# Performance work log

Hardware: AMD Instinct MI355X
Metric: run time of the kernel (lower is better)

The kernel has to match this reference:

```python
import jax, jax.numpy as jnp
import numpy as np

N = 50000          # num nodes
E = 800000         # num edges (avg degree 16)
D_IN, D_H, D_OUT = 128, 64, 64
HS, NC = 128, 10   # lstm hidden_size, num_classes


def setup_inputs() -> dict:
    key = jax.random.key(0)
    ks = jax.random.split(key, 20)
    s = 0.05
    rn = lambda k, shape: (jax.random.normal(k, shape, dtype=jnp.float32) * s)
    inp = {
        "x": jax.random.normal(ks[0], (N, D_IN), dtype=jnp.float32),
        "edge_index": jax.random.randint(ks[1], (2, E), 0, N, dtype=jnp.int64),
        # GCN layer weights (PyG GCNConv: lin has no bias; separate additive bias)
        "W1": rn(ks[2], (D_IN, D_H)), "b1": jnp.zeros((D_H,), jnp.float32),
        "W2": rn(ks[3], (D_H, D_H)), "b2": jnp.zeros((D_H,), jnp.float32),
        "W3": rn(ks[4], (D_H, D_H)), "b3": jnp.zeros((D_H,), jnp.float32),
        "W4": rn(ks[5], (D_H, D_H)), "b4": jnp.zeros((D_H,), jnp.float32),
        "W5": rn(ks[6], (D_H, D_OUT)), "b5": jnp.zeros((D_OUT,), jnp.float32),
        # LSTM (gate order i, f, g, o as in torch.nn.LSTM)
        "W_ih": rn(ks[7], (4 * HS, D_OUT)), "W_hh": rn(ks[8], (4 * HS, HS)),
        "b_ih": jnp.zeros((4 * HS,), jnp.float32), "b_hh": jnp.zeros((4 * HS,), jnp.float32),
        # FC head
        "W_fc": rn(ks[9], (NC, HS)), "b_fc": jnp.zeros((NC,), jnp.float32),
    }
    return inp


def reference(x, edge_index, W1, b1, W2, b2, W3, b3, W4, b4, W5, b5,
              W_ih, W_hh, b_ih, b_hh, W_fc, b_fc):
    n = x.shape[0]
    # add self loops (PyG GCNConv default)
    loops = jnp.arange(n, dtype=edge_index.dtype)
    row = jnp.concatenate([edge_index[0], loops])  # source nodes
    col = jnp.concatenate([edge_index[1], loops])  # target nodes
    # symmetric normalization D^{-1/2} (A+I) D^{-1/2}
    deg = jax.ops.segment_sum(jnp.ones_like(col, dtype=x.dtype), col, num_segments=n)
    dinv = jnp.where(deg > 0, jax.lax.rsqrt(deg), 0.0)
    norm = dinv[row] * dinv[col]                   # [E+N]

    def conv(h, W, b):
        h = h @ W                                  # [N, d_out]
        msg = h[row] * norm[:, None]               # gather + scale  [E+N, d_out]
        return jax.ops.segment_sum(msg, col, num_segments=n) + b

    h = jax.nn.relu(conv(x, W1, b1))
    h = jax.nn.relu(conv(h, W2, b2))
    h = jax.nn.relu(conv(h, W3, b3))
    h = jax.nn.relu(conv(h, W4, b4))
    h = jax.nn.relu(conv(h, W5, b5))               # [N, D_OUT]

    # single-timestep LSTM (seq_len=1, batch=N, h0=c0=0), gate order i,f,g,o
    hs = W_hh.shape[1]
    h0 = jnp.zeros((n, hs), x.dtype)
    c0 = jnp.zeros((n, hs), x.dtype)
    gates = h @ W_ih.T + h0 @ W_hh.T + b_ih + b_hh  # [N, 4*HS]
    i, f, g, o = jnp.split(gates, 4, axis=1)
    i = jax.nn.sigmoid(i); f = jax.nn.sigmoid(f)
    g = jnp.tanh(g);       o = jax.nn.sigmoid(o)
    c1 = f * c0 + i * g
    h1 = o * jnp.tanh(c1)                           # [N, HS]
    return h1 @ W_fc.T + b_fc                       # [N, NC]
```

## Files before the change

### kernel.cpp

```cpp
#include <hip/hip_runtime.h>
#include <math.h>

#define DOUT 64


__global__ __launch_bounds__(256) void k_count(const int* __restrict__ col,
                                               int* __restrict__ cnt, int e) {
    int i = blockIdx.x * 256 + threadIdx.x;
    if (i < e) atomicAdd(&cnt[col[i]], 1);
}


__global__ __launch_bounds__(256) void k_scanA(const int* __restrict__ cnt,
                                               int* __restrict__ bsum, int n) {
    __shared__ int part[256];
    const int t = threadIdx.x;
    const int base = blockIdx.x * 1024 + t * 4;
    int s = 0;
    #pragma unroll
    for (int i = 0; i < 4; i++) { int idx = base + i; if (idx < n) s += cnt[idx]; }
    part[t] = s;
    __syncthreads();
    #pragma unroll
    for (int off = 128; off > 0; off >>= 1) {
        if (t < off) part[t] += part[t + off];
        __syncthreads();
    }
    if (t == 0) bsum[blockIdx.x] = part[0];
}

__global__ __launch_bounds__(64) void k_scanB(const int* __restrict__ bsum,
                                              int* __restrict__ boff, int nb) {
    const int t = threadIdx.x;
    int val = (t < nb) ? bsum[t] : 0;
    const int own = val;
    #pragma unroll
    for (int off = 1; off < 64; off <<= 1) {
        int v = __shfl_up(val, off);
        if (t >= off) val += v;
    }
    if (t < nb) boff[t] = val - own;
}

__global__ __launch_bounds__(256) void k_scanC(const int* __restrict__ cnt,
                                               const int* __restrict__ boff,
                                               int* __restrict__ rowptr,
                                               int* __restrict__ cursor,
                                               float* __restrict__ dinv,
                                               int n, int e_total) {
    __shared__ int part[256];
    const int t = threadIdx.x;
    const int base = blockIdx.x * 1024 + t * 4;
    int c[4];
    int s = 0;
    #pragma unroll
    for (int i = 0; i < 4; i++) {
        int idx = base + i;
        c[i] = (idx < n) ? cnt[idx] : 0;
        s += c[i];
    }
    part[t] = s;
    __syncthreads();
    for (int off = 1; off < 256; off <<= 1) {
        int v = 0;
        if (t >= off) v = part[t - off];
        __syncthreads();
        if (t >= off) part[t] += v;
        __syncthreads();
    }
    int run = boff[blockIdx.x] + ((t > 0) ? part[t - 1] : 0);
    #pragma unroll
    for (int i = 0; i < 4; i++) {
        int idx = base + i;
        if (idx < n) {
            rowptr[idx] = run;
            cursor[idx] = run;
            dinv[idx] = rsqrtf((float)(c[i] + 1));
            run += c[i];
        }
    }
    if (blockIdx.x == 0 && t == 0) rowptr[n] = e_total;
}

__global__ __launch_bounds__(256) void k_fill(const int* __restrict__ row,
                                              const int* __restrict__ col,
                                              int* __restrict__ cursor,
                                              int* __restrict__ srcidx, int e) {
    int i = blockIdx.x * 256 + threadIdx.x;
    if (i < e) {
        int p = atomicAdd(&cursor[col[i]], 1);
        srcidx[p] = row[i];
    }
}

__global__ __launch_bounds__(256) void k_transp(const float* __restrict__ W1,
                                                const float* __restrict__ W2,
                                                const float* __restrict__ W3,
                                                const float* __restrict__ W4,
                                                const float* __restrict__ W5,
                                                float* __restrict__ WT) {
    int i = blockIdx.x * 256 + threadIdx.x;
    if (i < 8192) {
        int j = i >> 7, d = i & 127;
        WT[i] = W1[d * 64 + j];
    } else if (i < 24576) {
        int q = i - 8192;
        int w = q >> 12, r = q & 4095;
        int j = r >> 6, d = r & 63;
        const float* Ws = (w == 0) ? W2 : (w == 1) ? W3 : (w == 2) ? W4 : W5;
        WT[i] = Ws[d * 64 + j];
    }
}

template<int D, bool RELU>
__global__ __launch_bounds__(256) void k_gemm2(const float* __restrict__ X,
                                               const float* __restrict__ WT,
                                               const float* __restrict__ dinv,
                                               float* __restrict__ hWs, int n) {
    constexpr int D4 = D / 4;
    __shared__ float Wls[64 * D];
    __shared__ float Xls[32 * D];
    const int t = threadIdx.x;
    const int node0 = blockIdx.x * 32;
    float4* Wl4 = (float4*)Wls;
    float4* Xl4 = (float4*)Xls;

    for (int i = t; i < 64 * D4; i += 256) {
        int r = i / D4, d4 = i % D4;
        Wl4[r * D4 + (d4 ^ (((r >> 4) & 3) << 2))] = ((const float4*)WT)[i];
    }
    for (int i = t; i < 32 * D4; i += 256) {
        int nd = i / D4, d4 = i % D4;
        float4 v = make_float4(0.f, 0.f, 0.f, 0.f);
        int node = node0 + nd;
        if (node < n) {
            v = ((const float4*)X)[(size_t)node * D4 + d4];
            if (RELU) {
                v.x = fmaxf(v.x, 0.f); v.y = fmaxf(v.y, 0.f);
                v.z = fmaxf(v.z, 0.f); v.w = fmaxf(v.w, 0.f);
            }
            float di = dinv[node];
            v.x *= di; v.y *= di; v.z *= di; v.w *= di;
        }
        Xl4[i] = v;
    }
    __syncthreads();

    const int wv = t >> 6, lane = t & 63;
    const int swz = ((lane >> 4) & 3) << 2;
    float acc[8];
    #pragma unroll
    for (int q = 0; q < 8; q++) acc[q] = 0.f;

    #pragma unroll 4
    for (int d4 = 0; d4 < D4; d4++) {
        float4 w = Wl4[lane * D4 + (d4 ^ swz)];
        #pragma unroll
        for (int q = 0; q < 8; q++) {
            float4 xv = Xl4[(wv * 8 + q) * D4 + d4];
            acc[q] = fmaf(xv.w, w.w, fmaf(xv.z, w.z, fmaf(xv.y, w.y, fmaf(xv.x, w.x, acc[q]))));
        }
    }
    #pragma unroll
    for (int q = 0; q < 8; q++) {
        int node = node0 + wv * 8 + q;
        if (node < n) hWs[(size_t)node * 64 + lane] = acc[q];
    }
}

__global__ __launch_bounds__(256) void k_gather(const int* __restrict__ rowptr,
                                                const int* __restrict__ srcidx,
                                                const float* __restrict__ dinv,
                                                const float* __restrict__ b,
                                                const float* __restrict__ hWs,
                                                float* __restrict__ agg, int n) {
    const int t = threadIdx.x;
    int w = (blockIdx.x * 256 + t) >> 6;
    if (w >= n) return;
    w = __builtin_amdgcn_readfirstlane(w);
    const int lane = t & 63;
    const int f4 = lane & 15;
    const int es = lane >> 4;
    const float4* H4 = (const float4*)hWs;
    const int s = rowptr[w], e = rowptr[w + 1];
    float4 acc = make_float4(0.f, 0.f, 0.f, 0.f);
    if (es == 0) acc = H4[(size_t)w * 16 + f4];
    for (int i = s + es; i < e; i += 4) {
        int src = srcidx[i];
        float4 v = H4[(size_t)src * 16 + f4];
        acc.x += v.x; acc.y += v.y; acc.z += v.z; acc.w += v.w;
    }
    #pragma unroll
    for (int off = 16; off < 64; off <<= 1) {
        acc.x += __shfl_xor(acc.x, off);
        acc.y += __shfl_xor(acc.y, off);
        acc.z += __shfl_xor(acc.z, off);
        acc.w += __shfl_xor(acc.w, off);
    }
    if (es == 0) {
        float di = dinv[w];
        float4 bv = ((const float4*)b)[f4];
        float4 o;
        o.x = fmaf(acc.x, di, bv.x);
        o.y = fmaf(acc.y, di, bv.y);
        o.z = fmaf(acc.z, di, bv.z);
        o.w = fmaf(acc.w, di, bv.w);
        ((float4*)agg)[(size_t)w * 16 + f4] = o;
    }
}

__device__ __forceinline__ float sigm(float x) { return 1.f / (1.f + __expf(-x)); }
__device__ __forceinline__ float tanhf_(float x) { return 1.f - 2.f / (__expf(2.f * x) + 1.f); }

__global__ __launch_bounds__(256) void k_lstm_fc(const float* __restrict__ agg,
                                                 const float* __restrict__ W_ih,
                                                 const float* __restrict__ b_ih,
                                                 const float* __restrict__ b_hh,
                                                 const float* __restrict__ W_fc,
                                                 const float* __restrict__ b_fc,
                                                 float* __restrict__ out, int n) {
    __shared__ float smem[10240];
    float4* Wl4 = (float4*)smem;
    float4* hN4 = (float4*)(smem + 8192);
    const int t = threadIdx.x;
    const int wv = t >> 6, lane = t & 63;
    const int node0 = blockIdx.x * 32;
    const float4* A4 = (const float4*)agg;
    const float4* Wih4 = (const float4*)W_ih;

    const float bi0 = b_ih[lane]       + b_hh[lane];
    const float bi1 = b_ih[64 + lane]  + b_hh[64 + lane];
    const float bg0 = b_ih[256 + lane] + b_hh[256 + lane];
    const float bg1 = b_ih[320 + lane] + b_hh[320 + lane];
    const float bo0 = b_ih[384 + lane] + b_hh[384 + lane];
    const float bo1 = b_ih[448 + lane] + b_hh[448 + lane];

    for (int i = t; i < 512; i += 256) {
        int nd = i >> 4;
        float4 v = make_float4(0.f, 0.f, 0.f, 0.f);
        if (node0 + nd < n) {
            v = A4[(size_t)(node0 + nd) * 16 + (i & 15)];
            v.x = fmaxf(v.x, 0.f); v.y = fmaxf(v.y, 0.f);
            v.z = fmaxf(v.z, 0.f); v.w = fmaxf(v.w, 0.f);
        }
        hN4[i] = v;
    }

    float ac[3][2][8];
    #pragma unroll
    for (int g = 0; g < 3; g++)
        #pragma unroll
        for (int h = 0; h < 2; h++)
            #pragma unroll
            for (int q = 0; q < 8; q++) ac[g][h][q] = 0.f;

    const int sw = lane & 7;
    #pragma unroll
    for (int g = 0; g < 3; g++) {
        __syncthreads();
        const int grow0 = (g == 0) ? 0 : ((g + 1) * 128);
        for (int i = t; i < 2048; i += 256) {
            int r = i >> 4, d4 = i & 15;
            Wl4[(r << 4) | (d4 ^ (r & 7))] = Wih4[(size_t)(grow0 + r) * 16 + d4];
        }
        __syncthreads();
        #pragma unroll 2
        for (int j = 0; j < 16; j++) {
            int js = j ^ sw;
            float4 w0 = Wl4[(lane << 4) | js];
            float4 w1 = Wl4[((64 + lane) << 4) | js];
            #pragma unroll
            for (int q = 0; q < 8; q++) {
                float4 hv = hN4[((wv * 8 + q) << 4) | j];
                ac[g][0][q] = fmaf(hv.w, w0.w, fmaf(hv.z, w0.z, fmaf(hv.y, w0.y, fmaf(hv.x, w0.x, ac[g][0][q]))));
                ac[g][1][q] = fmaf(hv.w, w1.w, fmaf(hv.z, w1.z, fmaf(hv.y, w1.y, fmaf(hv.x, w1.x, ac[g][1][q]))));
            }
        }
    }

    __syncthreads();

    #pragma unroll
    for (int q = 0; q < 8; q++) {
        int nd = wv * 8 + q;
        float gi0 = ac[0][0][q] + bi0, gg0 = ac[1][0][q] + bg0, go0 = ac[2][0][q] + bo0;
        float gi1 = ac[0][1][q] + bi1, gg1 = ac[1][1][q] + bg1, go1 = ac[2][1][q] + bo1;
        float h1a = sigm(go0) * tanhf_(sigm(gi0) * tanhf_(gg0));
        float h1b = sigm(go1) * tanhf_(sigm(gi1) * tanhf_(gg1));
        smem[nd * 132 + lane]      = h1a;
        smem[nd * 132 + 64 + lane] = h1b;
    }
    float* wfcs = smem + 4224;
    for (int i = t; i < 1280; i += 256) wfcs[i] = W_fc[i];
    __syncthreads();

    for (int oc = t; oc < 320; oc += 256) {
        int nd = oc & 31, c = oc >> 5;
        const float4* hrow = (const float4*)&smem[nd * 132];
        const float4* wrow = (const float4*)&wfcs[c * 128];
        float s = 0.f;
        #pragma unroll 8
        for (int k4 = 0; k4 < 32; k4++) {
            float4 h = hrow[k4], w = wrow[k4];
            s = fmaf(h.w, w.w, fmaf(h.z, w.z, fmaf(h.y, w.y, fmaf(h.x, w.x, s))));
        }
        int node = node0 + nd;
        if (node < n) out[(size_t)node * 10 + c] = s + b_fc[c];
    }
}

extern "C" void kernel_launch(void* const* d_in, const int* in_sizes, int n_in,
                              void* d_out, int out_size, void* d_ws, size_t ws_size,
                              hipStream_t stream) {
    const float* x    = (const float*)d_in[0];
    const int*   ei   = (const int*)d_in[1];
    const float* W1   = (const float*)d_in[2];
    const float* b1   = (const float*)d_in[3];
    const float* W2   = (const float*)d_in[4];
    const float* b2   = (const float*)d_in[5];
    const float* W3   = (const float*)d_in[6];
    const float* b3   = (const float*)d_in[7];
    const float* W4   = (const float*)d_in[8];
    const float* b4   = (const float*)d_in[9];
    const float* W5   = (const float*)d_in[10];
    const float* b5   = (const float*)d_in[11];
    const float* W_ih = (const float*)d_in[12];
    const float* b_ih = (const float*)d_in[14];
    const float* b_hh = (const float*)d_in[15];
    const float* W_fc = (const float*)d_in[16];
    const float* b_fc = (const float*)d_in[17];
    float* out = (float*)d_out;

    const int N = in_sizes[0] / 128;
    const int E = in_sizes[1] / 2;
    const int* row = ei;
    const int* col = ei + E;

    size_t off = 0;
    auto alloc = [&](size_t elems) { size_t cur = off; off += (elems + 3) & ~(size_t)3; return cur; };
    int*   base_i = (int*)d_ws;
    float* base_f = (float*)d_ws;
    int*   cnt    = base_i + alloc(N);
    int*   rowptr = base_i + alloc((size_t)N + 1);
    int*   cursor = base_i + alloc(N);
    int*   srcidx = base_i + alloc(E);
    int*   bsum   = base_i + alloc(64);
    int*   boff   = base_i + alloc(64);
    float* dinv   = base_f + alloc(N);
    float* WT     = base_f + alloc(24576);
    float* hWs    = base_f + alloc((size_t)N * 64);
    float* agg    = base_f + alloc((size_t)N * 64);
    float* WT1 = WT;
    float* WT2 = WT + 8192;
    float* WT3 = WT + 8192 + 4096;
    float* WT4 = WT + 8192 + 8192;
    float* WT5 = WT + 8192 + 12288;

    const int nbE  = (E + 255) / 256;
    const int nbGa = (N * 64 + 255) / 256;
    const int nbGe = (N + 31) / 32;
    const int nbL  = (N + 31) / 32;
    const int nbS  = (N + 1023) / 1024;

    hipMemsetAsync(cnt, 0, sizeof(int) * N, stream);
    k_transp<<<96, 256, 0, stream>>>(W1, W2, W3, W4, W5, WT);
    k_count<<<nbE, 256, 0, stream>>>(col, cnt, E);
    k_scanA<<<nbS, 256, 0, stream>>>(cnt, bsum, N);
    k_scanB<<<1, 64, 0, stream>>>(bsum, boff, nbS);
    k_scanC<<<nbS, 256, 0, stream>>>(cnt, boff, rowptr, cursor, dinv, N, E);
    k_fill<<<nbE, 256, 0, stream>>>(row, col, cursor, srcidx, E);

    k_gemm2<128, false><<<nbGe, 256, 0, stream>>>(x, WT1, dinv, hWs, N);
    k_gather<<<nbGa, 256, 0, stream>>>(rowptr, srcidx, dinv, b1, hWs, agg, N);
    k_gemm2<64, true><<<nbGe, 256, 0, stream>>>(agg, WT2, dinv, hWs, N);
    k_gather<<<nbGa, 256, 0, stream>>>(rowptr, srcidx, dinv, b2, hWs, agg, N);
    k_gemm2<64, true><<<nbGe, 256, 0, stream>>>(agg, WT3, dinv, hWs, N);
    k_gather<<<nbGa, 256, 0, stream>>>(rowptr, srcidx, dinv, b3, hWs, agg, N);
    k_gemm2<64, true><<<nbGe, 256, 0, stream>>>(agg, WT4, dinv, hWs, N);
    k_gather<<<nbGa, 256, 0, stream>>>(rowptr, srcidx, dinv, b4, hWs, agg, N);
    k_gemm2<64, true><<<nbGe, 256, 0, stream>>>(agg, WT5, dinv, hWs, N);
    k_gather<<<nbGa, 256, 0, stream>>>(rowptr, srcidx, dinv, b5, hWs, agg, N);

    k_lstm_fc<<<nbL, 256, 0, stream>>>(agg, W_ih, b_ih, b_hh, W_fc, b_fc, out, N);
}
```

Baseline: 592.2 us.

## Store hidden features in quarter-split planar layout for cache-local gathers

Hidden features are stored as four column slabs of 16 features each (slab-major, then node) instead of row-major 64-wide rows. Each gather block now handles one slab, so a slab's random source-row reads cover a quarter of the data and are more likely to hit in L2/MALL. Each wave processes 16 edges in parallel with 4 lanes per row instead of 4 edges with 16 lanes. The GEMM and LSTM kernels are updated to read and write the new layout, and the LDS swizzle pattern is changed. The trade-off is that rowptr and srcidx are now read four times, and each gathered row segment is only 64 bytes.

```diff
diff --git a/kernel.cpp b/kernel.cpp
--- a/kernel.cpp
+++ b/kernel.cpp
@@ -112,7 +112,7 @@
     }
 }
 
-template<int D, bool RELU>
+template<int D, bool RELU, bool QIN>
 __global__ __launch_bounds__(256) void k_gemm2(const float* __restrict__ X,
                                                const float* __restrict__ WT,
                                                const float* __restrict__ dinv,
@@ -127,14 +127,18 @@
 
     for (int i = t; i < 64 * D4; i += 256) {
         int r = i / D4, d4 = i % D4;
-        Wl4[r * D4 + (d4 ^ (((r >> 4) & 3) << 2))] = ((const float4*)WT)[i];
+        Wl4[r * D4 + (d4 ^ (r & 7))] = ((const float4*)WT)[i];
     }
     for (int i = t; i < 32 * D4; i += 256) {
         int nd = i / D4, d4 = i % D4;
         float4 v = make_float4(0.f, 0.f, 0.f, 0.f);
         int node = node0 + nd;
         if (node < n) {
-            v = ((const float4*)X)[(size_t)node * D4 + d4];
+            if (QIN) {
+                v = ((const float4*)X)[((size_t)((d4 >> 2) * n + node)) * 4 + (d4 & 3)];
+            } else {
+                v = ((const float4*)X)[(size_t)node * D4 + d4];
+            }
             if (RELU) {
                 v.x = fmaxf(v.x, 0.f); v.y = fmaxf(v.y, 0.f);
                 v.z = fmaxf(v.z, 0.f); v.w = fmaxf(v.w, 0.f);
@@ -147,24 +151,25 @@
     __syncthreads();
 
     const int wv = t >> 6, lane = t & 63;
-    const int swz = ((lane >> 4) & 3) << 2;
+    const int sw = lane & 7;
     float acc[8];
     #pragma unroll
     for (int q = 0; q < 8; q++) acc[q] = 0.f;
 
     #pragma unroll 4
     for (int d4 = 0; d4 < D4; d4++) {
-        float4 w = Wl4[lane * D4 + (d4 ^ swz)];
+        float4 w = Wl4[lane * D4 + (d4 ^ sw)];
         #pragma unroll
         for (int q = 0; q < 8; q++) {
             float4 xv = Xl4[(wv * 8 + q) * D4 + d4];
             acc[q] = fmaf(xv.w, w.w, fmaf(xv.z, w.z, fmaf(xv.y, w.y, fmaf(xv.x, w.x, acc[q]))));
         }
     }
+    const int qj = lane >> 4, jc = lane & 15;
     #pragma unroll
     for (int q = 0; q < 8; q++) {
         int node = node0 + wv * 8 + q;
-        if (node < n) hWs[(size_t)node * 64 + lane] = acc[q];
+        if (node < n) hWs[((size_t)(qj * n + node)) * 16 + jc] = acc[q];
     }
 }
 
@@ -173,25 +178,27 @@
                                                 const float* __restrict__ dinv,
                                                 const float* __restrict__ b,
                                                 const float* __restrict__ hWs,
-                                                float* __restrict__ agg, int n) {
-    const int t = threadIdx.x;
-    int w = (blockIdx.x * 256 + t) >> 6;
+                                                float* __restrict__ agg,
+                                                int n, int bpq) {
+    const int t = threadIdx.x;
+    const int q = blockIdx.x / bpq;
+    int w = (blockIdx.x - q * bpq) * 4 + (t >> 6);
     if (w >= n) return;
     w = __builtin_amdgcn_readfirstlane(w);
     const int lane = t & 63;
-    const int f4 = lane & 15;
-    const int es = lane >> 4;
-    const float4* H4 = (const float4*)hWs;
+    const int f4 = lane & 3;
+    const int es = lane >> 2;
+    const float4* H4 = (const float4*)hWs + (size_t)q * n * 4;
     const int s = rowptr[w], e = rowptr[w + 1];
     float4 acc = make_float4(0.f, 0.f, 0.f, 0.f);
-    if (es == 0) acc = H4[(size_t)w * 16 + f4];
-    for (int i = s + es; i < e; i += 4) {
+    if (es == 0) acc = H4[(size_t)w * 4 + f4];
+    for (int i = s + es; i < e; i += 16) {
         int src = srcidx[i];
-        float4 v = H4[(size_t)src * 16 + f4];
+        float4 v = H4[(size_t)src * 4 + f4];
         acc.x += v.x; acc.y += v.y; acc.z += v.z; acc.w += v.w;
     }
     #pragma unroll
-    for (int off = 16; off < 64; off <<= 1) {
+    for (int off = 4; off < 64; off <<= 1) {
         acc.x += __shfl_xor(acc.x, off);
         acc.y += __shfl_xor(acc.y, off);
         acc.z += __shfl_xor(acc.z, off);
@@ -199,13 +206,13 @@
     }
     if (es == 0) {
         float di = dinv[w];
-        float4 bv = ((const float4*)b)[f4];
+        float4 bv = ((const float4*)b)[q * 4 + f4];
         float4 o;
         o.x = fmaf(acc.x, di, bv.x);
         o.y = fmaf(acc.y, di, bv.y);
         o.z = fmaf(acc.z, di, bv.z);
         o.w = fmaf(acc.w, di, bv.w);
-        ((float4*)agg)[(size_t)w * 16 + f4] = o;
+        ((float4*)agg)[((size_t)(q * n + w)) * 4 + f4] = o;
     }
 }
 
@@ -236,10 +243,11 @@
     const float bo1 = b_ih[448 + lane] + b_hh[448 + lane];
 
     for (int i = t; i < 512; i += 256) {
-        int nd = i >> 4;
+        int nd = i >> 4, f4i = i & 15;
         float4 v = make_float4(0.f, 0.f, 0.f, 0.f);
-        if (node0 + nd < n) {
-            v = A4[(size_t)(node0 + nd) * 16 + (i & 15)];
+        int node = node0 + nd;
+        if (node < n) {
+            v = A4[((size_t)((f4i >> 2) * n + node)) * 4 + (f4i & 3)];
             v.x = fmaxf(v.x, 0.f); v.y = fmaxf(v.y, 0.f);
             v.z = fmaxf(v.z, 0.f); v.w = fmaxf(v.w, 0.f);
         }
@@ -357,7 +365,8 @@
     float* WT5 = WT + 8192 + 12288;
 
     const int nbE  = (E + 255) / 256;
-    const int nbGa = (N * 64 + 255) / 256;
+    const int bpq  = (N + 3) / 4;
+    const int nbGa = 4 * bpq;
     const int nbGe = (N + 31) / 32;
     const int nbL  = (N + 31) / 32;
     const int nbS  = (N + 1023) / 1024;
@@ -370,16 +379,16 @@
     k_scanC<<<nbS, 256, 0, stream>>>(cnt, boff, rowptr, cursor, dinv, N, E);
     k_fill<<<nbE, 256, 0, stream>>>(row, col, cursor, srcidx, E);
 
-    k_gemm2<128, false><<<nbGe, 256, 0, stream>>>(x, WT1, dinv, hWs, N);
-    k_gather<<<nbGa, 256, 0, stream>>>(rowptr, srcidx, dinv, b1, hWs, agg, N);
-    k_gemm2<64, true><<<nbGe, 256, 0, stream>>>(agg, WT2, dinv, hWs, N);
-    k_gather<<<nbGa, 256, 0, stream>>>(rowptr, srcidx, dinv, b2, hWs, agg, N);
-    k_gemm2<64, true><<<nbGe, 256, 0, stream>>>(agg, WT3, dinv, hWs, N);
-    k_gather<<<nbGa, 256, 0, stream>>>(rowptr, srcidx, dinv, b3, hWs, agg, N);
-    k_gemm2<64, true><<<nbGe, 256, 0, stream>>>(agg, WT4, dinv, hWs, N);
-    k_gather<<<nbGa, 256, 0, stream>>>(rowptr, srcidx, dinv, b4, hWs, agg, N);
-    k_gemm2<64, true><<<nbGe, 256, 0, stream>>>(agg, WT5, dinv, hWs, N);
-    k_gather<<<nbGa, 256, 0, stream>>>(rowptr, srcidx, dinv, b5, hWs, agg, N);
+    k_gemm2<128, false, false><<<nbGe, 256, 0, stream>>>(x, WT1, dinv, hWs, N);
+    k_gather<<<nbGa, 256, 0, stream>>>(rowptr, srcidx, dinv, b1, hWs, agg, N, bpq);
+    k_gemm2<64, true, true><<<nbGe, 256, 0, stream>>>(agg, WT2, dinv, hWs, N);
+    k_gather<<<nbGa, 256, 0, stream>>>(rowptr, srcidx, dinv, b2, hWs, agg, N, bpq);
+    k_gemm2<64, true, true><<<nbGe, 256, 0, stream>>>(agg, WT3, dinv, hWs, N);
+    k_gather<<<nbGa, 256, 0, stream>>>(rowptr, srcidx, dinv, b3, hWs, agg, N, bpq);
+    k_gemm2<64, true, true><<<nbGe, 256, 0, stream>>>(agg, WT4, dinv, hWs, N);
+    k_gather<<<nbGa, 256, 0, stream>>>(rowptr, srcidx, dinv, b4, hWs, agg, N, bpq);
+    k_gemm2<64, true, true><<<nbGe, 256, 0, stream>>>(agg, WT5, dinv, hWs, N);
+    k_gather<<<nbGa, 256, 0, stream>>>(rowptr, srcidx, dinv, b5, hWs, agg, N, bpq);
 
     k_lstm_fc<<<nbL, 256, 0, stream>>>(agg, W_ih, b_ih, b_hh, W_fc, b_fc, out, N);
 }
```

New measurement: 657.6 us. +11.1%, slower.
